# Optimization experiments

Hardware: AMD Instinct MI355X
Metric: run time of the kernel (lower is better)

Reference implementation:

```python
import jax, jax.numpy as jnp
import numpy as np

EPS_NORM = 1e-6
EPS_MM = 1e-5


def feature_l2norm(f, axis=1):
    # torch: f / sqrt(sum(f^2, dim) + 1e-6)
    return f / jnp.sqrt(jnp.sum(f * f, axis=axis, keepdims=True) + EPS_NORM)


def mutual_matching(c):
    # c: [b, 1, f1, f2, f3, f4]
    b, ch, f1, f2, f3, f4 = c.shape
    # max over (f1,f2) for each (f3,f4) target location
    max_B = jnp.max(c.reshape(b, f1 * f2, f3, f4), axis=1).reshape(b, 1, 1, 1, f3, f4)
    # max over (f3,f4) for each (f1,f2) source location
    max_A = jnp.max(c.reshape(b, f1 * f2, f3 * f4), axis=2).reshape(b, 1, f1, f2, 1, 1)
    return c * (c / (max_A + EPS_MM)) * (c / (max_B + EPS_MM))


def correlation4d(fa, fb):
    # fa: [b,c,hA,wA], fb: [b,c,hB,wB] -> [b,1,hA,wA,hB,wB]
    corr = jnp.einsum('bcij,bckl->bijkl', fa, fb)[:, None]
    corr = jax.nn.relu(corr)
    return feature_l2norm(corr, axis=1)  # channel dim is 1 -> x/sqrt(x^2+eps)


def conv4d(x, w, b):
    # x: [B,Ci,f1,f2,f3,f4]; w: [Co,Ci,k,k,k,k]; b: [Co]
    # Implemented as a sum of k 3D convs over (f2,f3,f4), sliding along f1 --
    # exactly the Conv4d emulation used by NC-Net.
    B, Ci, f1, f2, f3, f4 = x.shape
    Co, _, k = w.shape[:3]
    p = k // 2
    xp = jnp.pad(x, ((0, 0), (0, 0), (p, p), (0, 0), (0, 0), (0, 0)))
    out = None
    for i in range(k):
        xi = jax.lax.dynamic_slice_in_dim(xp, i, f1, axis=2)        # [B,Ci,f1,f2,f3,f4]
        xi = xi.transpose(0, 2, 1, 3, 4, 5).reshape(B * f1, Ci, f2, f3, f4)
        yi = jax.lax.conv_general_dilated(
            xi, w[:, :, i], window_strides=(1, 1, 1),
            padding=[(p, p)] * 3,
            dimension_numbers=('NCDHW', 'OIDHW', 'NCDHW'))
        yi = yi.reshape(B, f1, Co, f2, f3, f4).transpose(0, 2, 1, 3, 4, 5)
        out = yi if out is None else out + yi
    return out + b[None, :, None, None, None, None]


def nc_stack(x, params):
    # Sequential(Conv4d, ReLU) x 3
    for w, b in params:
        x = jax.nn.relu(conv4d(x, w, b))
    return x


def neigh_consensus(x, params):
    # symmetric mode: conv(x) + conv(x.permute(0,1,4,5,2,3)).permute back
    ya = nc_stack(x, params)
    yb = nc_stack(x.transpose(0, 1, 4, 5, 2, 3), params).transpose(0, 1, 4, 5, 2, 3)
    return ya + yb


def setup_inputs() -> dict:
    key = jax.random.key(0)
    ks = jax.random.split(key, 8)
    b, c, h, w = 4, 256, 32, 32
    feature_A = jax.random.normal(ks[0], (b, c, h, w), dtype=jnp.float32)
    feature_B = jax.random.normal(ks[1], (b, c, h, w), dtype=jnp.float32)
    k = 3
    w1 = jax.random.normal(ks[2], (10, 1, k, k, k, k), dtype=jnp.float32) * 0.05
    b1 = jnp.zeros((10,), jnp.float32)
    w2 = jax.random.normal(ks[3], (10, 10, k, k, k, k), dtype=jnp.float32) * 0.05
    b2 = jnp.zeros((10,), jnp.float32)
    w3 = jax.random.normal(ks[4], (1, 10, k, k, k, k), dtype=jnp.float32) * 0.05
    b3 = jnp.zeros((1,), jnp.float32)
    return {"feature_A": feature_A, "feature_B": feature_B,
            "w1": w1, "b1": b1, "w2": w2, "b2": b2, "w3": w3, "b3": b3}


def reference(feature_A, feature_B, w1, b1, w2, b2, w3, b3):
    fa = feature_l2norm(feature_A, axis=1)
    fb = feature_l2norm(feature_B, axis=1)
    corr4d = correlation4d(fa, fb)                   # [b,1,hA,wA,hB,wB]
    corr4d = mutual_matching(corr4d)
    corr4d = neigh_consensus(corr4d, [(w1, b1), (w2, b2), (w3, b3)])
    corr4d = mutual_matching(corr4d)
    return corr4d
```

## Files before the change

### kernel.cpp

```cpp
#include <hip/hip_runtime.h>

#define EPSN 1e-6f
#define EPSM 1e-5f

typedef __fp16 h2v __attribute__((ext_vector_type(2)));
typedef __fp16 f16x4 __attribute__((ext_vector_type(4)));
typedef float f32x4 __attribute__((ext_vector_type(4)));

#define MFMA16(a, b, c) __builtin_amdgcn_mfma_f32_16x16x16f16((a), (b), (c), 0, 0, 0)

__device__ __forceinline__ unsigned pkh2(float a, float b) {
    union { h2v h; unsigned u; } v;
    v.h = __builtin_amdgcn_cvt_pkrtz(a, b);
    return v.u;
}

__device__ __forceinline__ float dot2f(unsigned a, unsigned b, float c) {
    union { unsigned u; h2v h; } ua, ub;
    ua.u = a; ub.u = b;
#if __has_builtin(__builtin_amdgcn_fdot2)
    return __builtin_amdgcn_fdot2(ua.h, ub.h, c, false);
#else
    return fmaf((float)ua.h.x, (float)ub.h.x,
                fmaf((float)ua.h.y, (float)ub.h.y, c));
#endif
}

__global__ __launch_bounds__(256) void invnorm_k(const float* __restrict__ f,
                                                 float* __restrict__ inv)
{
    int pbase = blockIdx.x * 64;
    int pp = threadIdx.x & 63;
    int cc = threadIdx.x >> 6;
    int pos = pbase + pp;
    int b = pos >> 10, ij = pos & 1023;
    const float* fp = f + (size_t)(b * 256) * 1024 + ij;
    float s = 0.f;
    #pragma unroll 8
    for (int k = 0; k < 64; ++k) {
        float v = fp[(size_t)(cc * 64 + k) * 1024];
        s += v * v;
    }
    __shared__ float red[4][64];
    red[cc][pp] = s;
    __syncthreads();
    if (cc == 0) {
        float t = red[0][pp] + red[1][pp] + red[2][pp] + red[3][pp];
        inv[pos] = rsqrtf(t + EPSN);
    }
}

__global__ __launch_bounds__(256) void corr_k(const float* __restrict__ fa,
                                              const float* __restrict__ fb,
                                              const float* __restrict__ invA,
                                              const float* __restrict__ invB,
                                              float* __restrict__ corr)
{
    __shared__ float As[16][68];
    __shared__ float Bs[16][68];
    int b = blockIdx.z;
    int i0 = blockIdx.y * 64, j0 = blockIdx.x * 64;
    int tid = threadIdx.x;
    int tx = tid & 15, ty = tid >> 4;
    const float* fab = fa + (size_t)b * 256 * 1024;
    const float* fbb = fb + (size_t)b * 256 * 1024;
    const float* ia = invA + b * 1024 + i0;
    const float* ib = invB + b * 1024 + j0;
    float acc[4][4] = {};
    for (int kc = 0; kc < 256; kc += 16) {
        #pragma unroll
        for (int l = 0; l < 4; ++l) {
            int idx = tid + l * 256;
            int r = idx >> 6, cix = idx & 63;
            As[r][cix] = fab[(size_t)(kc + r) * 1024 + i0 + cix] * ia[cix];
            Bs[r][cix] = fbb[(size_t)(kc + r) * 1024 + j0 + cix] * ib[cix];
        }
        __syncthreads();
        #pragma unroll
        for (int k = 0; k < 16; ++k) {
            float4 av = *(const float4*)&As[k][ty * 4];
            float4 bv = *(const float4*)&Bs[k][tx * 4];
            float a[4] = {av.x, av.y, av.z, av.w};
            float bq[4] = {bv.x, bv.y, bv.z, bv.w};
            #pragma unroll
            for (int ii = 0; ii < 4; ++ii)
                #pragma unroll
                for (int jj = 0; jj < 4; ++jj)
                    acc[ii][jj] += a[ii] * bq[jj];
        }
        __syncthreads();
    }
    float* cb = corr + ((size_t)b << 20);
    #pragma unroll
    for (int ii = 0; ii < 4; ++ii) {
        float4 o; float v;
        v = fmaxf(acc[ii][0], 0.f); o.x = v * rsqrtf(v * v + EPSN);
        v = fmaxf(acc[ii][1], 0.f); o.y = v * rsqrtf(v * v + EPSN);
        v = fmaxf(acc[ii][2], 0.f); o.z = v * rsqrtf(v * v + EPSN);
        v = fmaxf(acc[ii][3], 0.f); o.w = v * rsqrtf(v * v + EPSN);
        *(float4*)&cb[(size_t)(i0 + ty * 4 + ii) * 1024 + j0 + tx * 4] = o;
    }
}

__global__ __launch_bounds__(256) void rowmax_k(const float* __restrict__ c,
                                                float* __restrict__ maxR)
{
    int b = blockIdx.y, i = blockIdx.x, tid = threadIdx.x;
    const float* row = c + ((size_t)b << 20) + ((size_t)i << 10);
    float m = fmaxf(fmaxf(row[tid], row[tid + 256]), fmaxf(row[tid + 512], row[tid + 768]));
    #pragma unroll
    for (int off = 32; off; off >>= 1) m = fmaxf(m, __shfl_down(m, off, 64));
    __shared__ float sred[4];
    if ((tid & 63) == 0) sred[tid >> 6] = m;
    __syncthreads();
    if (tid == 0)
        maxR[b * 1024 + i] = fmaxf(fmaxf(sred[0], sred[1]), fmaxf(sred[2], sred[3]));
}

__global__ __launch_bounds__(256) void colmax_k(const float* __restrict__ c,
                                                float* __restrict__ maxC)
{
    int j = blockIdx.x * 256 + threadIdx.x;
    int r0 = blockIdx.y * 128;
    int b = blockIdx.z;
    const float* cb = c + ((size_t)b << 20);
    float m = 0.f;
    for (int r = 0; r < 128; ++r) m = fmaxf(m, cb[(size_t)(r0 + r) * 1024 + j]);
    atomicMax((int*)&maxC[b * 1024 + j], __float_as_int(m));
}

__global__ __launch_bounds__(256) void mmapply_k(float* __restrict__ c,
                                                 const float* __restrict__ maxR,
                                                 const float* __restrict__ maxC)
{
    int e4 = blockIdx.x * 256 + threadIdx.x;
    int e = e4 * 4;
    int b = e >> 20, i = (e >> 10) & 1023, j0 = e & 1023;
    float4 v = ((float4*)c)[e4];
    float ra = 1.f / (maxR[b * 1024 + i] + EPSM);
    float4 mb = ((const float4*)maxC)[(b * 1024 + j0) >> 2];
    float4 o;
    o.x = v.x * v.x * v.x * ra / (mb.x + EPSM);
    o.y = v.y * v.y * v.y * ra / (mb.y + EPSM);
    o.z = v.z * v.z * v.z * ra / (mb.z + EPSM);
    o.w = v.w * v.w * v.w * ra / (mb.w + EPSM);
    ((float4*)c)[e4] = o;
}

template <int CI, int CO>
__global__ void packw_k(const float* __restrict__ w, float* __restrict__ dst, int perm)
{
    constexpr int WS = (3 * CO + 3) & ~3;
    int idx = blockIdx.x * 256 + threadIdx.x;
    if (idx >= CI * 27 * WS) return;
    int ci = idx / (27 * WS);
    int rem = idx - ci * 27 * WS;
    int d123 = rem / WS;
    int slot = rem - d123 * WS;
    float v = 0.f;
    if (slot < 3 * CO) {
        int d4 = slot / CO, co = slot - d4 * CO;
        int t = d123 * 3 + d4;
        int d1 = t / 27, r2 = t % 27;
        int d2 = r2 / 9, r3 = r2 % 9;
        int d3 = r3 / 3, dd4 = r3 % 3;
        int st = perm ? (d3 * 27 + dd4 * 9 + d1 * 3 + d2) : t;
        v = w[(co * CI + ci) * 81 + st];
    }
    dst[idx] = v;
}

__global__ void packwm_k(const float* __restrict__ w, unsigned short* __restrict__ dst,
                         int perm)
{
    int idx = blockIdx.x * 256 + threadIdx.x;
    if (idx >= 20736) return;
    int tap = idx >> 8;
    int co  = (idx >> 4) & 15;
    int k   = idx & 15;
    float v = 0.f;
    if (co < 10 && k < 10) {
        int d1 = tap / 27, r2 = tap % 27;
        int d2 = r2 / 9, r3 = r2 % 9;
        int d3 = r3 / 3, d4 = r3 % 3;
        int st = perm ? (d3 * 27 + d4 * 9 + d1 * 3 + d2) : tap;
        v = w[(co * 10 + k) * 81 + st];
    }
    union { __fp16 h; unsigned short u; } cv;
    cv.h = (__fp16)v;
    dst[idx] = cv.u;
}

template <int CIP, int CO>
__global__ void packw2_k(const float* __restrict__ w, unsigned* __restrict__ dst, int perm)
{
    constexpr int WS = (3 * CO + 3) & ~3;
    int idx = blockIdx.x * 256 + threadIdx.x;
    if (idx >= CIP * 27 * WS) return;
    int pp = idx / (27 * WS);
    int rem = idx - pp * 27 * WS;
    int d123 = rem / WS;
    int slot = rem - d123 * WS;
    unsigned v = 0u;
    if (slot < 3 * CO) {
        int d4 = slot / CO, co = slot - d4 * CO;
        int t = d123 * 3 + d4;
        int d1 = t / 27, r2 = t % 27;
        int d2 = r2 / 9, r3 = r2 % 9;
        int d3 = r3 / 3, dd4 = r3 % 3;
        int st = perm ? (d3 * 27 + dd4 * 9 + d1 * 3 + d2) : t;
        float f0 = w[(co * 2 * CIP + 2 * pp) * 81 + st];
        float f1 = w[(co * 2 * CIP + 2 * pp + 1) * 81 + st];
        v = pkh2(f0, f1);
    }
    dst[idx] = v;
}

template <int CI, int CO, bool ADD, bool PACK>
__global__ __launch_bounds__(256, 4) void conv4d_k(const float* __restrict__ x,
                                                   const float* __restrict__ wp,
                                                   const float* __restrict__ bias,
                                                   float* __restrict__ y)
{
    constexpr int WS = (3 * CO + 3) & ~3;
    constexpr int NW4 = WS / 4;
    constexpr int SLAB = 34 * 35;
    __shared__ float tile[3 * SLAB];

    int tid = threadIdx.x;
    int f1 = blockIdx.x >> 5, f2 = blockIdx.x & 31;
    int q = tid & 7, yy = tid >> 3;
    int x0 = q << 2;

    for (int e = tid; e < 3 * SLAB; e += 256) tile[e] = 0.f;

    float acc[CO][4];
    #pragma unroll
    for (int co = 0; co < CO; ++co) {
        float bv = bias[co];
        acc[co][0] = bv; acc[co][1] = bv; acc[co][2] = bv; acc[co][3] = bv;
    }

    float bufA[WS], bufB[WS];

#define TAP(U, WB, WN, PF) do {                                               \
        constexpr int u_ = (U);                                               \
        const float* rowb_ = &tile[(u_/3)*SLAB + (yy + u_%3)*35 + x0];        \
        float xs_[6];                                                         \
        _Pragma("unroll") for (int j = 0; j < 6; ++j) xs_[j] = rowb_[j];      \
        if (PF) {                                                             \
            _Pragma("unroll") for (int k = 0; k < NW4; ++k)                   \
                *(float4*)&WN[k*4] =                                          \
                    ((const float4*)(wphase + (u_+1)*WS))[k];                 \
        }                                                                     \
        _Pragma("unroll") for (int d4 = 0; d4 < 3; ++d4)                      \
        _Pragma("unroll") for (int co = 0; co < CO; ++co) {                   \
            float wf_ = WB[d4*CO + co];                                       \
            _Pragma("unroll") for (int p = 0; p < 4; ++p)                     \
                acc[co][p] = fmaf(xs_[p + d4], wf_, acc[co][p]);              \
        }                                                                     \
    } while (0)

    #pragma unroll 1
    for (int ci = 0; ci < CI; ++ci) {
        const float* wci = wp + ci * 27 * WS;
        #pragma unroll 1
        for (int d1 = 0; d1 < 3; ++d1) {
            int g1 = f1 + d1 - 1;
            bool g1ok = (unsigned)g1 < 32u;
            const float* wphase = wci + d1 * 9 * WS;
            __syncthreads();
            #pragma unroll
            for (int k = 0; k < NW4; ++k)
                *(float4*)&bufA[k*4] = ((const float4*)wphase)[k];
            #pragma unroll
            for (int it = 0; it < 3; ++it) {
                int e = tid + it * 256;
                int s2 = e >> 8, rr = (e >> 3) & 31, qq = e & 7;
                int g2 = f2 + s2 - 1;
                float4 v = {0.f, 0.f, 0.f, 0.f};
                if (g1ok & ((unsigned)g2 < 32u))
                    v = *(const float4*)&x[((size_t)ci << 20) +
                        ((size_t)((g1 << 5) + g2) << 10) + (rr << 5) + (qq << 2)];
                float* t = &tile[s2 * SLAB + (rr + 1) * 35 + 1 + (qq << 2)];
                t[0] = v.x; t[1] = v.y; t[2] = v.z; t[3] = v.w;
            }
            __syncthreads();

            TAP(0, bufA, bufB, true);
            TAP(1, bufB, bufA, true);
            TAP(2, bufA, bufB, true);
            TAP(3, bufB, bufA, true);
            TAP(4, bufA, bufB, true);
            TAP(5, bufB, bufA, true);
            TAP(6, bufA, bufB, true);
            TAP(7, bufB, bufA, true);
            TAP(8, bufA, bufB, false);
        }
    }
#undef TAP

    size_t obase = ((size_t)(f1 * 32 + f2) << 10) + yy * 32 + x0;
    if (PACK) {
        unsigned* ypu = (unsigned*)y;
        #pragma unroll
        for (int c = 0; c < CO / 2; ++c) {
            uint4 o;
            o.x = pkh2(fmaxf(acc[2*c][0], 0.f), fmaxf(acc[2*c+1][0], 0.f));
            o.y = pkh2(fmaxf(acc[2*c][1], 0.f), fmaxf(acc[2*c+1][1], 0.f));
            o.z = pkh2(fmaxf(acc[2*c][2], 0.f), fmaxf(acc[2*c+1][2], 0.f));
            o.w = pkh2(fmaxf(acc[2*c][3], 0.f), fmaxf(acc[2*c+1][3], 0.f));
            *(uint4*)&ypu[(size_t)c * 1048576 + obase] = o;
        }
    } else {
        #pragma unroll
        for (int co = 0; co < CO; ++co) {
            float4 o;
            o.x = fmaxf(acc[co][0], 0.f);
            o.y = fmaxf(acc[co][1], 0.f);
            o.z = fmaxf(acc[co][2], 0.f);
            o.w = fmaxf(acc[co][3], 0.f);
            float* yp = y + ((size_t)co << 20) + obase;
            if (ADD) {
                float4 prev = *(const float4*)yp;
                o.x += prev.x; o.y += prev.y; o.z += prev.z; o.w += prev.w;
            }
            *(float4*)yp = o;
        }
    }
}

__global__ __launch_bounds__(256, 4) void conv4dm_k(const unsigned* __restrict__ xp,
                                                    const unsigned short* __restrict__ wm,
                                                    const float* __restrict__ bias,
                                                    unsigned* __restrict__ yp)
{
    __shared__ unsigned tile[3 * 10 * 34 * 9];

    int tid = threadIdx.x;
    int bx = blockIdx.x;
    int q  = bx & 3;
    int f2 = (bx >> 2) & 31;
    int f1 = bx >> 7;
    int l  = tid & 63;
    int wv = tid >> 6;
    int sl = l & 15;
    int g  = l >> 4;

    for (int e = tid; e < 9180; e += 256) tile[e] = 0u;

    f32x4 bv;
    #pragma unroll
    for (int e = 0; e < 4; ++e) {
        int co = 4 * g + e;
        bv[e] = (co < 10) ? bias[co] : 0.f;
    }
    f32x4 acc0 = bv, acc1 = bv, acc2 = bv, acc3 = bv;

    int qbase = q * 8;

    #pragma unroll 1
    for (int d1 = 0; d1 < 3; ++d1) {
        int g1 = f1 + d1 - 1;
        bool g1ok = (unsigned)g1 < 32u;
        __syncthreads();

        uint2 aw[27];
        #pragma unroll
        for (int t27 = 0; t27 < 27; ++t27) {
            int tap = d1 * 27 + t27;
            aw[t27] = *(const uint2*)&wm[(tap << 8) + (sl << 4) + (g << 2)];
        }

        #pragma unroll
        for (int it = 0; it < 4; ++it) {
            int e = tid + it * 256;
            if (e < 960) {
                int c  = (e & 31) + 1;
                int rg = e >> 5;
                int r  = rg % 10;
                int s2 = rg / 10;
                int g2 = f2 + s2 - 1;
                int g3 = qbase + r - 1;
                unsigned v0 = 0, v1 = 0, v2 = 0, v3 = 0, v4 = 0;
                if (g1ok & ((unsigned)g2 < 32u) & ((unsigned)g3 < 32u)) {
                    size_t off = ((size_t)((g1 << 5) + g2) << 10) + (g3 << 5) + (c - 1);
                    v0 = xp[off];
                    v1 = xp[off + 1048576];
                    v2 = xp[off + 2097152];
                    v3 = xp[off + 3145728];
                    v4 = xp[off + 4194304];
                }
                unsigned* t = &tile[((s2 * 10 + r) * 34 + c) * 9];
                t[0] = v0; t[1] = v1; t[2] = v2; t[3] = v3; t[4] = v4;
            }
        }
        __syncthreads();

        int tb0 = ((wv * 2 + 0) * 34 + sl) * 9 + (g << 1);
        #pragma unroll
        for (int d2 = 0; d2 < 3; ++d2)
        #pragma unroll
        for (int d3 = 0; d3 < 3; ++d3)
        #pragma unroll
        for (int d4 = 0; d4 < 3; ++d4) {
            int t27 = d2 * 9 + d3 * 3 + d4;
            union { uint2 u; f16x4 h; } A; A.u = aw[t27];
            int tapoff = ((d2 * 10 + d3) * 34 + d4) * 9;
            const unsigned* bp = &tile[tb0 + tapoff];
            union { uint2 u; f16x4 h; } B;
            B.u.x = bp[0];           B.u.y = bp[1];
            acc0 = MFMA16(A.h, B.h, acc0);
            B.u.x = bp[16 * 9];      B.u.y = bp[16 * 9 + 1];
            acc1 = MFMA16(A.h, B.h, acc1);
            B.u.x = bp[34 * 9];      B.u.y = bp[34 * 9 + 1];
            acc2 = MFMA16(A.h, B.h, acc2);
            B.u.x = bp[50 * 9];      B.u.y = bp[50 * 9 + 1];
            acc3 = MFMA16(A.h, B.h, acc3);
        }
    }

    size_t pbase = ((size_t)((f1 << 5) + f2) << 10);
#define STORE_TILE(ACC, RT, CH) do {                                          \
        size_t sidx = pbase + ((size_t)(qbase + (RT)) << 5) + (CH) * 16 + sl; \
        float r0 = fmaxf((ACC)[0], 0.f), r1 = fmaxf((ACC)[1], 0.f);           \
        float r2 = fmaxf((ACC)[2], 0.f), r3 = fmaxf((ACC)[3], 0.f);           \
        if (g < 2) {                                                          \
            yp[(size_t)(2 * g)     * 1048576 + sidx] = pkh2(r0, r1);          \
            yp[(size_t)(2 * g + 1) * 1048576 + sidx] = pkh2(r2, r3);          \
        } else if (g == 2) {                                                  \
            yp[(size_t)4 * 1048576 + sidx] = pkh2(r0, r1);                    \
        }                                                                     \
    } while (0)
    STORE_TILE(acc0, wv * 2 + 0, 0);
    STORE_TILE(acc1, wv * 2 + 0, 1);
    STORE_TILE(acc2, wv * 2 + 1, 0);
    STORE_TILE(acc3, wv * 2 + 1, 1);
#undef STORE_TILE
}

template <int CIP, int CO, bool ADD>
__global__ __launch_bounds__(256, 4) void conv4dp_k(const unsigned* __restrict__ xp,
                                                    const unsigned* __restrict__ wp,
                                                    const float* __restrict__ bias,
                                                    float* __restrict__ y)
{
    constexpr int WS = (3 * CO + 3) & ~3;
    constexpr int NW4 = WS / 4;
    constexpr int SLAB = 34 * 35;
    __shared__ unsigned tile[3 * SLAB];

    int tid = threadIdx.x;
    int f1 = blockIdx.x >> 5, f2 = blockIdx.x & 31;
    int q = tid & 7, yy = tid >> 3;
    int x0 = q << 2;

    for (int e = tid; e < 3 * SLAB; e += 256) tile[e] = 0u;

    float acc[CO][4];
    #pragma unroll
    for (int co = 0; co < CO; ++co) {
        float bvv = bias[co];
        acc[co][0] = bvv; acc[co][1] = bvv; acc[co][2] = bvv; acc[co][3] = bvv;
    }

    unsigned bufA[WS], bufB[WS];

#define TAPP(U, WB, WN, PF) do {                                              \
        constexpr int u_ = (U);                                               \
        const unsigned* rowb_ = &tile[(u_/3)*SLAB + (yy + u_%3)*35 + x0];     \
        unsigned xs_[6];                                                      \
        _Pragma("unroll") for (int j = 0; j < 6; ++j) xs_[j] = rowb_[j];      \
        if (PF) {                                                             \
            _Pragma("unroll") for (int k = 0; k < NW4; ++k)                   \
                *(uint4*)&WN[k*4] =                                           \
                    ((const uint4*)(wphase + (u_+1)*WS))[k];                  \
        }                                                                     \
        _Pragma("unroll") for (int d4 = 0; d4 < 3; ++d4)                      \
        _Pragma("unroll") for (int co = 0; co < CO; ++co) {                   \
            unsigned wf_ = WB[d4*CO + co];                                    \
            _Pragma("unroll") for (int p = 0; p < 4; ++p)                     \
                acc[co][p] = dot2f(xs_[p + d4], wf_, acc[co][p]);             \
        }                                                                     \
    } while (0)

    #pragma unroll 1
    for (int pp = 0; pp < CIP; ++pp) {
        const unsigned* wci = wp + pp * 27 * WS;
        #pragma unroll 1
        for (int d1 = 0; d1 < 3; ++d1) {
            int g1 = f1 + d1 - 1;
            bool g1ok = (unsigned)g1 < 32u;
            const unsigned* wphase = wci + d1 * 9 * WS;
            __syncthreads();
            #pragma unroll
            for (int k = 0; k < NW4; ++k)
                *(uint4*)&bufA[k*4] = ((const uint4*)wphase)[k];
            #pragma unroll
            for (int it = 0; it < 3; ++it) {
                int e = tid + it * 256;
                int s2 = e >> 8, rr = (e >> 3) & 31, qq = e & 7;
                int g2 = f2 + s2 - 1;
                uint4 v = {0u, 0u, 0u, 0u};
                if (g1ok & ((unsigned)g2 < 32u))
                    v = *(const uint4*)&xp[((size_t)pp << 20) +
                        ((size_t)((g1 << 5) + g2) << 10) + (rr << 5) + (qq << 2)];
                unsigned* t = &tile[s2 * SLAB + (rr + 1) * 35 + 1 + (qq << 2)];
                t[0] = v.x; t[1] = v.y; t[2] = v.z; t[3] = v.w;
            }
            __syncthreads();

            TAPP(0, bufA, bufB, true);
            TAPP(1, bufB, bufA, true);
            TAPP(2, bufA, bufB, true);
            TAPP(3, bufB, bufA, true);
            TAPP(4, bufA, bufB, true);
            TAPP(5, bufB, bufA, true);
            TAPP(6, bufA, bufB, true);
            TAPP(7, bufB, bufA, true);
            TAPP(8, bufA, bufB, false);
        }
    }
#undef TAPP

    size_t obase = ((size_t)(f1 * 32 + f2) << 10) + yy * 32 + x0;
    #pragma unroll
    for (int co = 0; co < CO; ++co) {
        float4 o;
        o.x = fmaxf(acc[co][0], 0.f);
        o.y = fmaxf(acc[co][1], 0.f);
        o.z = fmaxf(acc[co][2], 0.f);
        o.w = fmaxf(acc[co][3], 0.f);
        float* ypt = y + ((size_t)co << 20) + obase;
        if (ADD) {
            float4 prev = *(const float4*)ypt;
            o.x += prev.x; o.y += prev.y; o.z += prev.z; o.w += prev.w;
        }
        *(float4*)ypt = o;
    }
}

extern "C" void kernel_launch(void* const* d_in, const int* in_sizes, int n_in,
                              void* d_out, int out_size, void* d_ws, size_t ws_size,
                              hipStream_t stream)
{
    (void)in_sizes; (void)n_in; (void)out_size; (void)ws_size;
    const float* fA = (const float*)d_in[0];
    const float* fB = (const float*)d_in[1];
    const float* w1 = (const float*)d_in[2];
    const float* b1 = (const float*)d_in[3];
    const float* w2 = (const float*)d_in[4];
    const float* b2 = (const float*)d_in[5];
    const float* w3 = (const float*)d_in[6];
    const float* b3 = (const float*)d_in[7];
    float* out = (float*)d_out;
    float* ws = (float*)d_ws;

    size_t o = 0;
    float* invA = ws + o; o += 4096;
    float* invB = ws + o; o += 4096;
    float* maxR = ws + o; o += 4096;
    float* maxC = ws + o; o += 4096;
    float* pw1  = ws + o; o += 2048;
    unsigned short* wm2 = (unsigned short*)(ws + o); o += 20736;
    unsigned* pw3 = (unsigned*)(ws + o); o += 1080;
    float* corr = ws + o; o += 4194304;
    unsigned* t1p = (unsigned*)(ws + o); o += 5242880;
    unsigned* t2p = (unsigned*)(ws + o); o += 5242880;

    invnorm_k<<<64, 256, 0, stream>>>(fA, invA);
    invnorm_k<<<64, 256, 0, stream>>>(fB, invB);
    corr_k<<<dim3(16, 16, 4), 256, 0, stream>>>(fA, fB, invA, invB, corr);

    rowmax_k<<<dim3(1024, 4), 256, 0, stream>>>(corr, maxR);
    (void)hipMemsetAsync(maxC, 0, 4096 * sizeof(float), stream);
    colmax_k<<<dim3(4, 8, 4), 256, 0, stream>>>(corr, maxC);
    mmapply_k<<<4096, 256, 0, stream>>>(corr, maxR, maxC);

    packw_k<1, 10><<<4, 256, 0, stream>>>(w1, pw1, 0);
    packw_k<1, 10><<<4, 256, 0, stream>>>(w1, pw1 + 864, 1);
    packwm_k<<<81, 256, 0, stream>>>(w2, wm2, 0);
    packwm_k<<<81, 256, 0, stream>>>(w2, wm2 + 20736, 1);
    packw2_k<5, 1><<<3, 256, 0, stream>>>(w3, pw3, 0);
    packw2_k<5, 1><<<3, 256, 0, stream>>>(w3, pw3 + 540, 1);

    for (int b = 0; b < 4; ++b) {
        const float* xb = corr + (size_t)b * 1048576;
        float* ob = out + (size_t)b * 1048576;
        conv4d_k<1, 10, false, true><<<1024, 256, 0, stream>>>(xb, pw1, b1, (float*)t1p);
        conv4dm_k<<<4096, 256, 0, stream>>>(t1p, wm2, b2, t2p);
        conv4dp_k<5, 1, false><<<1024, 256, 0, stream>>>(t2p, pw3, b3, ob);
        conv4d_k<1, 10, false, true><<<1024, 256, 0, stream>>>(xb, pw1 + 864, b1, (float*)t1p);
        conv4dm_k<<<4096, 256, 0, stream>>>(t1p, wm2 + 20736, b2, t2p);
        conv4dp_k<5, 1, true ><<<1024, 256, 0, stream>>>(t2p, pw3 + 540, b3, ob);
    }

    rowmax_k<<<dim3(1024, 4), 256, 0, stream>>>(out, maxR);
    (void)hipMemsetAsync(maxC, 0, 4096 * sizeof(float), stream);
    colmax_k<<<dim3(4, 8, 4), 256, 0, stream>>>(out, maxC);
    mmapply_k<<<4096, 256, 0, stream>>>(out, maxR, maxC);
}
```

Measured before the change: 1.659 ms.

## Vectorize conv4dm tile loads, stage output through LDS, and remap block order

```diff
diff --git a/kernel.cpp b/kernel.cpp
--- a/kernel.cpp
+++ b/kernel.cpp
@@ -339,9 +339,12 @@
 
     int tid = threadIdx.x;
     int bx = blockIdx.x;
-    int q  = bx & 3;
-    int f2 = (bx >> 2) & 31;
-    int f1 = bx >> 7;
+    int chunk  = bx & 7;
+    int within = bx >> 3;
+    int f1 = (chunk << 2) | (within >> 7);
+    int f2 = (within >> 2) & 31;
+    int q  = within & 3;
+
     int l  = tid & 63;
     int wv = tid >> 6;
     int sl = l & 15;
@@ -372,28 +375,30 @@
             aw[t27] = *(const uint2*)&wm[(tap << 8) + (sl << 4) + (g << 2)];
         }
 
-        #pragma unroll
-        for (int it = 0; it < 4; ++it) {
-            int e = tid + it * 256;
-            if (e < 960) {
-                int c  = (e & 31) + 1;
-                int rg = e >> 5;
-                int r  = rg % 10;
-                int s2 = rg / 10;
-                int g2 = f2 + s2 - 1;
-                int g3 = qbase + r - 1;
-                unsigned v0 = 0, v1 = 0, v2 = 0, v3 = 0, v4 = 0;
-                if (g1ok & ((unsigned)g2 < 32u) & ((unsigned)g3 < 32u)) {
-                    size_t off = ((size_t)((g1 << 5) + g2) << 10) + (g3 << 5) + (c - 1);
-                    v0 = xp[off];
-                    v1 = xp[off + 1048576];
-                    v2 = xp[off + 2097152];
-                    v3 = xp[off + 3145728];
-                    v4 = xp[off + 4194304];
-                }
-                unsigned* t = &tile[((s2 * 10 + r) * 34 + c) * 9];
-                t[0] = v0; t[1] = v1; t[2] = v2; t[3] = v3; t[4] = v4;
+        if (tid < 240) {
+            int k  = tid & 7;
+            int rg = tid >> 3;
+            int r  = rg % 10;
+            int s2 = rg / 10;
+            int c  = 1 + (k << 2);
+            int g2 = f2 + s2 - 1;
+            int g3 = qbase + r - 1;
+            uint4 v0 = {0,0,0,0}, v1 = {0,0,0,0}, v2 = {0,0,0,0},
+                  v3 = {0,0,0,0}, v4 = {0,0,0,0};
+            if (g1ok & ((unsigned)g2 < 32u) & ((unsigned)g3 < 32u)) {
+                size_t off = ((size_t)((g1 << 5) + g2) << 10) + (g3 << 5) + (c - 1);
+                v0 = *(const uint4*)&xp[off];
+                v1 = *(const uint4*)&xp[off + 1048576];
+                v2 = *(const uint4*)&xp[off + 2097152];
+                v3 = *(const uint4*)&xp[off + 3145728];
+                v4 = *(const uint4*)&xp[off + 4194304];
             }
+            unsigned* tb = &tile[((s2 * 10 + r) * 34 + c) * 9];
+            tb[0] = v0.x; tb[9]  = v0.y; tb[18] = v0.z; tb[27] = v0.w;
+            tb[1] = v1.x; tb[10] = v1.y; tb[19] = v1.z; tb[28] = v1.w;
+            tb[2] = v2.x; tb[11] = v2.y; tb[20] = v2.z; tb[29] = v2.w;
+            tb[3] = v3.x; tb[12] = v3.y; tb[21] = v3.z; tb[30] = v3.w;
+            tb[4] = v4.x; tb[13] = v4.y; tb[22] = v4.z; tb[31] = v4.w;
         }
         __syncthreads();
 
@@ -420,23 +425,39 @@
         }
     }
 
-    size_t pbase = ((size_t)((f1 << 5) + f2) << 10);
-#define STORE_TILE(ACC, RT, CH) do {                                          \
-        size_t sidx = pbase + ((size_t)(qbase + (RT)) << 5) + (CH) * 16 + sl; \
+    __syncthreads();
+#define EPST(ACC, RT, CH) do {                                                \
+        int row_ = (RT);                                                      \
+        int col_ = (CH) * 16 + sl;                                            \
         float r0 = fmaxf((ACC)[0], 0.f), r1 = fmaxf((ACC)[1], 0.f);           \
         float r2 = fmaxf((ACC)[2], 0.f), r3 = fmaxf((ACC)[3], 0.f);           \
         if (g < 2) {                                                          \
-            yp[(size_t)(2 * g)     * 1048576 + sidx] = pkh2(r0, r1);          \
-            yp[(size_t)(2 * g + 1) * 1048576 + sidx] = pkh2(r2, r3);          \
+            tile[((2*g)     * 8 + row_) * 33 + col_] = pkh2(r0, r1);          \
+            tile[((2*g + 1) * 8 + row_) * 33 + col_] = pkh2(r2, r3);          \
         } else if (g == 2) {                                                  \
-            yp[(size_t)4 * 1048576 + sidx] = pkh2(r0, r1);                    \
+            tile[(4 * 8 + row_) * 33 + col_] = pkh2(r0, r1);                  \
         }                                                                     \
     } while (0)
-    STORE_TILE(acc0, wv * 2 + 0, 0);
-    STORE_TILE(acc1, wv * 2 + 0, 1);
-    STORE_TILE(acc2, wv * 2 + 1, 0);
-    STORE_TILE(acc3, wv * 2 + 1, 1);
-#undef STORE_TILE
+    EPST(acc0, wv * 2 + 0, 0);
+    EPST(acc1, wv * 2 + 0, 1);
+    EPST(acc2, wv * 2 + 1, 0);
+    EPST(acc3, wv * 2 + 1, 1);
+#undef EPST
+    __syncthreads();
+
+    size_t pbase = ((size_t)((f1 << 5) + f2) << 10);
+    #pragma unroll
+    for (int u = tid; u < 320; u += 256) {
+        int p   = u >> 6;
+        int rem = u & 63;
+        int row = rem >> 3;
+        int cg  = rem & 7;
+        const unsigned* src = &tile[(p * 8 + row) * 33 + (cg << 2)];
+        uint4 v;
+        v.x = src[0]; v.y = src[1]; v.z = src[2]; v.w = src[3];
+        *(uint4*)&yp[(size_t)p * 1048576 + pbase +
+                     ((size_t)(qbase + row) << 5) + (cg << 2)] = v;
+    }
 }
 
 template <int CIP, int CO, bool ADD>
```

Result: faster. 1.565 ms (-5.7%).
